# Performance work log

Hardware: AMD Instinct MI355X
Metric: run time of the kernel (lower is better)

The kernel has to match this reference:

```python
import jax, jax.numpy as jnp
import numpy as np

ROUTINGS = 3
NUM_CAPSULE = 32
DIM_CAPSULE = 64


def squash(x, axis=-1):
    # scale = sqrt(||x||^2 + eps) / (0.5 + ||x||^2 + eps)
    sq = jnp.sum(x * x, axis=axis, keepdims=True) + 1e-7
    return (jnp.sqrt(sq) / (0.5 + sq)) * x


def setup_inputs() -> dict:
    key = jax.random.key(0)
    k1, k2 = jax.random.split(key)
    B, IN, ID = 64, 1024, 256
    u_vecs = jax.random.normal(k1, (B, IN, ID), dtype=jnp.float32)
    # nn.Linear weight [NC*DC, ID], xavier_normal init
    fan_out, fan_in = NUM_CAPSULE * DIM_CAPSULE, ID
    std = np.sqrt(2.0 / (fan_in + fan_out)).astype(np.float32)
    W = jax.random.normal(k2, (fan_out, fan_in), dtype=jnp.float32) * std
    return {"u_vecs": u_vecs, "W": W}


def reference(u_vecs, W):
    B, IN, ID = u_vecs.shape
    # Linear projection: [B, IN, NC*DC]
    u_hat = jnp.einsum('bid,od->bio', u_vecs, W)
    # -> [B, NC, IN, DC]
    u_hat = u_hat.reshape(B, IN, NUM_CAPSULE, DIM_CAPSULE).transpose(0, 2, 1, 3)

    b = jnp.zeros((B, NUM_CAPSULE, IN), dtype=u_hat.dtype)
    o = None
    for i in range(ROUTINGS):
        c = jax.nn.softmax(b, axis=1)                      # softmax over output capsules
        o = jnp.einsum('bni,bnid->bnd', c, u_hat)          # [B, NC, DC]
        if i < ROUTINGS - 1:
            # F.normalize(o, 2, -1): x / max(||x||, 1e-12)
            norm = jnp.linalg.norm(o, axis=-1, keepdims=True)
            o = o / jnp.maximum(norm, 1e-12)
            b = jnp.einsum('bnid,bnd->bni', u_hat, o)
    return squash(o)
```

## Files before the change

kernel.cpp:

```cpp
#include <hip/hip_runtime.h>
#include <math.h>


#define B   64
#define IN  1024
#define ID  256
#define NC  32
#define DC  64

__global__ __launch_bounds__(256) void k_sumu(const float* __restrict__ u,
                                              float* __restrict__ sp0) {
    const int c = blockIdx.x, b = blockIdx.y;
    const int d = threadIdx.x;
    const float* up = u + ((size_t)b * IN + (size_t)c * (IN / 8)) * ID + d;
    float acc = 0.f;
#pragma unroll 8
    for (int i = 0; i < IN / 8; ++i) acc += up[(size_t)i * ID];
    sp0[(c * B + b) * ID + d] = acc;
}

__global__ __launch_bounds__(256) void k_ot(const float* __restrict__ W,
                                            const float* __restrict__ src,
                                            float* __restrict__ tout,
                                            const int mode) {
    const int bn = blockIdx.x;
    const int b = bn / NC, n = bn % NC;
    __shared__ float s_lds[ID];
    __shared__ float o_lds[DC];
    __shared__ float on_lds[DC];
    const int tid = threadIdx.x;

    float sv = 0.f;
    if (mode == 0) {
#pragma unroll
        for (int c = 0; c < 8; ++c) sv += src[(c * B + b) * ID + tid];
        sv *= (1.0f / NC);
    } else {
#pragma unroll
        for (int c = 0; c < 8; ++c) sv += src[((size_t)(c * B + b) * NC + n) * ID + tid];
    }
    s_lds[tid] = sv;
    __syncthreads();

    const int wave = tid >> 6, lane = tid & 63;
    const float* Wn = W + (size_t)n * DC * ID;
#pragma unroll 4
    for (int r = 0; r < 16; ++r) {
        const int d = wave * 16 + r;
        const float* wrow = Wn + (size_t)d * ID;
        float p = wrow[lane]        * s_lds[lane]
                + wrow[lane + 64]   * s_lds[lane + 64]
                + wrow[lane + 128]  * s_lds[lane + 128]
                + wrow[lane + 192]  * s_lds[lane + 192];
#pragma unroll
        for (int off = 32; off > 0; off >>= 1) p += __shfl_down(p, off);
        if (lane == 0) o_lds[d] = p;
    }
    __syncthreads();

    if (mode == 2) {
        if (tid < DC) {
            float v = o_lds[tid];
            float sq = v * v;
#pragma unroll
            for (int off = 32; off > 0; off >>= 1) sq += __shfl_down(sq, off);
            sq = __shfl(sq, 0) + 1e-7f;
            const float sc = sqrtf(sq) / (0.5f + sq);
            tout[(size_t)(b * NC + n) * DC + tid] = v * sc;
        }
        return;
    }

    if (tid < DC) {
        float v = o_lds[tid];
        float sq = v * v;
#pragma unroll
        for (int off = 32; off > 0; off >>= 1) sq += __shfl_down(sq, off);
        sq = __shfl(sq, 0);
        const float inv = 1.0f / fmaxf(sqrtf(sq), 1e-12f);
        on_lds[tid] = v * inv;
    }
    __syncthreads();

    float acc = 0.f;
    const float* wc = Wn + tid;
#pragma unroll 8
    for (int d = 0; d < DC; ++d) acc += wc[(size_t)d * ID] * on_lds[d];
    tout[((size_t)b * NC + n) * ID + tid] = acc;
}

#define RTILE 128
__global__ __launch_bounds__(256) void k_route(const float* __restrict__ u,
                                               const float* __restrict__ t,
                                               float* __restrict__ sp) {
    const int it = blockIdx.x, b = blockIdx.y;
    const int iBase = it * RTILE;
    __shared__ __align__(16) float Tst[NC][ID];
    __shared__ __align__(16) float Us[2][RTILE][20];
    __shared__ __align__(16) float cl[RTILE][36];
    const int tid = threadIdx.x;

    const float* ub = u + ((size_t)b * IN + iBase) * ID;
    const float* tb = t + (size_t)b * NC * ID;

#pragma unroll
    for (int rep = 0; rep < 8; ++rep) {
        const int idx = tid + rep * 256;
        const int n = idx >> 6, c4 = idx & 63;
        const float4 v = *(const float4*)(tb + (size_t)n * ID + c4 * 4);
        const int c_sw = (c4 * 4) ^ (((n >> 2) & 7) << 2);
        *(float4*)&Tst[n][c_sw] = v;
    }

    const int q = tid >> 3;
    const int r = tid & 7;
    const int i0 = q * 4, n0 = r * 4;
    const int si0 = tid >> 2,        sk0 = tid & 3;
    const int si1 = (tid + 256) >> 2, sk1 = (tid + 256) & 3;
    const int sc0 = 4 * (sk0 ^ ((si0 >> 2) & 3));
    const int sc1 = 4 * (sk1 ^ ((si1 >> 2) & 3));
    const int qs = q & 3;

    float acc[4][4] = {{0.f}};
    float4 pre0 = *(const float4*)(ub + (size_t)si0 * ID + sk0 * 4);
    float4 pre1 = *(const float4*)(ub + (size_t)si1 * ID + sk1 * 4);

    for (int kc = 0; kc < ID / 16; ++kc) {
        const int buf = kc & 1;
        *(float4*)&Us[buf][si0][sc0] = pre0;
        *(float4*)&Us[buf][si1][sc1] = pre1;
        __syncthreads();
        if (kc < ID / 16 - 1) {
            pre0 = *(const float4*)(ub + (size_t)si0 * ID + (kc + 1) * 16 + sk0 * 4);
            pre1 = *(const float4*)(ub + (size_t)si1 * ID + (kc + 1) * 16 + sk1 * 4);
        }
#pragma unroll
        for (int k4 = 0; k4 < 4; ++k4) {
            float4 a[4], bv[4];
            const int ac = 4 * (k4 ^ qs);
#pragma unroll
            for (int ii = 0; ii < 4; ++ii) a[ii] = *(const float4*)&Us[buf][i0 + ii][ac];
            const int bc = (kc * 16 + k4 * 4) ^ (r << 2);
#pragma unroll
            for (int jj = 0; jj < 4; ++jj) bv[jj] = *(const float4*)&Tst[n0 + jj][bc];
#pragma unroll
            for (int ii = 0; ii < 4; ++ii)
#pragma unroll
                for (int jj = 0; jj < 4; ++jj)
                    acc[ii][jj] += a[ii].x * bv[jj].x + a[ii].y * bv[jj].y
                                 + a[ii].z * bv[jj].z + a[ii].w * bv[jj].w;
        }
        __syncthreads();
    }

#pragma unroll
    for (int ii = 0; ii < 4; ++ii)
        *(float4*)&cl[i0 + ii][n0] =
            make_float4(acc[ii][0], acc[ii][1], acc[ii][2], acc[ii][3]);
    __syncthreads();

    {
        const int i = tid >> 1, half = tid & 1;
        float v[16];
#pragma unroll
        for (int j = 0; j < 16; ++j) v[j] = cl[i][half * 16 + j];
        float mx = v[0];
#pragma unroll
        for (int j = 1; j < 16; ++j) mx = fmaxf(mx, v[j]);
        mx = fmaxf(mx, __shfl_xor(mx, 1));
        float sum = 0.f;
#pragma unroll
        for (int j = 0; j < 16; ++j) { v[j] = __expf(v[j] - mx); sum += v[j]; }
        sum += __shfl_xor(sum, 1);
        const float inv = 1.0f / sum;
#pragma unroll
        for (int j = 0; j < 16; ++j) cl[i][half * 16 + j] = v[j] * inv;
    }
    __syncthreads();

    const int d4 = tid & 63;
    const int ng = tid >> 6;
    float a2[8][4] = {{0.f}};
    const float* ur = ub + d4 * 4;
#pragma unroll 4
    for (int i = 0; i < RTILE; ++i) {
        const float4 uv = *(const float4*)(ur + (size_t)i * ID);
        const float4 c0 = *(const float4*)&cl[i][ng * 8];
        const float4 c1 = *(const float4*)&cl[i][ng * 8 + 4];
        const float cv[8] = {c0.x, c0.y, c0.z, c0.w, c1.x, c1.y, c1.z, c1.w};
        const float uvv[4] = {uv.x, uv.y, uv.z, uv.w};
#pragma unroll
        for (int j = 0; j < 8; ++j)
#pragma unroll
            for (int x = 0; x < 4; ++x) a2[j][x] += cv[j] * uvv[x];
    }

    float* spb = sp + (size_t)(it * B + b) * NC * ID;
#pragma unroll
    for (int j = 0; j < 8; ++j) {
        const int n = ng * 8 + j;
        *(float4*)&spb[(size_t)n * ID + d4 * 4] =
            make_float4(a2[j][0], a2[j][1], a2[j][2], a2[j][3]);
    }
}

extern "C" void kernel_launch(void* const* d_in, const int* in_sizes, int n_in,
                              void* d_out, int out_size, void* d_ws, size_t ws_size,
                              hipStream_t stream) {
    const float* u = (const float*)d_in[0];
    const float* W = (const float*)d_in[1];
    float* out = (float*)d_out;

    float* ws  = (float*)d_ws;
    float* t   = ws;
    float* sp  = t + (size_t)B * NC * ID;
    float* sp0 = sp + (size_t)8 * B * NC * ID;

    k_sumu <<<dim3(8, B), dim3(256), 0, stream>>>(u, sp0);
    k_ot   <<<dim3(B * NC), dim3(256), 0, stream>>>(W, sp0, t, 0);
    k_route<<<dim3(IN / RTILE, B), dim3(256), 0, stream>>>(u, t, sp);
    k_ot   <<<dim3(B * NC), dim3(256), 0, stream>>>(W, sp, t, 1);
    k_route<<<dim3(IN / RTILE, B), dim3(256), 0, stream>>>(u, t, sp);
    k_ot   <<<dim3(B * NC), dim3(256), 0, stream>>>(W, sp, out, 2);
}
```

Measured before the change: 236.7 us.

## Read u directly from global in routing GEMM and alias shared buffers

The routing kernel no longer stages u tiles through a double-buffered shared-memory array with per-chunk barriers. Each thread now loads its four u rows directly from global memory as float4 and keeps only the T matrix in LDS. The logits buffer is aliased onto the same LDS as T, which cuts LDS use so more blocks can run per CU (launch bounds set to 4). The trade is uncoalesced, strided global loads of u that rely on L1/L2 caching instead of explicit LDS reuse across the eight threads sharing each row.

```diff
diff --git a/kernel.cpp b/kernel.cpp
--- a/kernel.cpp
+++ b/kernel.cpp
@@ -90,14 +90,14 @@
 }
 
 #define RTILE 128
-__global__ __launch_bounds__(256) void k_route(const float* __restrict__ u,
-                                               const float* __restrict__ t,
-                                               float* __restrict__ sp) {
+__global__ __launch_bounds__(256, 4) void k_route(const float* __restrict__ u,
+                                                  const float* __restrict__ t,
+                                                  float* __restrict__ sp) {
     const int it = blockIdx.x, b = blockIdx.y;
     const int iBase = it * RTILE;
-    __shared__ __align__(16) float Tst[NC][ID];
-    __shared__ __align__(16) float Us[2][RTILE][20];
-    __shared__ __align__(16) float cl[RTILE][36];
+    __shared__ __align__(16) float smem[NC * ID];
+    float (*Tst)[ID] = (float(*)[ID])smem;
+    float (*cl)[36]  = (float(*)[36])smem;
     const int tid = threadIdx.x;
 
     const float* ub = u + ((size_t)b * IN + iBase) * ID;
@@ -108,50 +108,39 @@
         const int idx = tid + rep * 256;
         const int n = idx >> 6, c4 = idx & 63;
         const float4 v = *(const float4*)(tb + (size_t)n * ID + c4 * 4);
-        const int c_sw = (c4 * 4) ^ (((n >> 2) & 7) << 2);
-        *(float4*)&Tst[n][c_sw] = v;
-    }
+        *(float4*)&Tst[n][(c4 * 4) ^ ((n >> 2) << 2)] = v;
+    }
+    __syncthreads();
 
     const int q = tid >> 3;
     const int r = tid & 7;
     const int i0 = q * 4, n0 = r * 4;
-    const int si0 = tid >> 2,        sk0 = tid & 3;
-    const int si1 = (tid + 256) >> 2, sk1 = (tid + 256) & 3;
-    const int sc0 = 4 * (sk0 ^ ((si0 >> 2) & 3));
-    const int sc1 = 4 * (sk1 ^ ((si1 >> 2) & 3));
-    const int qs = q & 3;
-
+    const int rsw = r << 2;
     float acc[4][4] = {{0.f}};
-    float4 pre0 = *(const float4*)(ub + (size_t)si0 * ID + sk0 * 4);
-    float4 pre1 = *(const float4*)(ub + (size_t)si1 * ID + sk1 * 4);
-
-    for (int kc = 0; kc < ID / 16; ++kc) {
-        const int buf = kc & 1;
-        *(float4*)&Us[buf][si0][sc0] = pre0;
-        *(float4*)&Us[buf][si1][sc1] = pre1;
-        __syncthreads();
-        if (kc < ID / 16 - 1) {
-            pre0 = *(const float4*)(ub + (size_t)si0 * ID + (kc + 1) * 16 + sk0 * 4);
-            pre1 = *(const float4*)(ub + (size_t)si1 * ID + (kc + 1) * 16 + sk1 * 4);
-        }
-#pragma unroll
-        for (int k4 = 0; k4 < 4; ++k4) {
-            float4 a[4], bv[4];
-            const int ac = 4 * (k4 ^ qs);
-#pragma unroll
-            for (int ii = 0; ii < 4; ++ii) a[ii] = *(const float4*)&Us[buf][i0 + ii][ac];
-            const int bc = (kc * 16 + k4 * 4) ^ (r << 2);
-#pragma unroll
-            for (int jj = 0; jj < 4; ++jj) bv[jj] = *(const float4*)&Tst[n0 + jj][bc];
-#pragma unroll
-            for (int ii = 0; ii < 4; ++ii)
-#pragma unroll
-                for (int jj = 0; jj < 4; ++jj)
-                    acc[ii][jj] += a[ii].x * bv[jj].x + a[ii].y * bv[jj].y
-                                 + a[ii].z * bv[jj].z + a[ii].w * bv[jj].w;
-        }
-        __syncthreads();
-    }
+    const float* up0 = ub + (size_t)(i0 + 0) * ID;
+    const float* up1 = ub + (size_t)(i0 + 1) * ID;
+    const float* up2 = ub + (size_t)(i0 + 2) * ID;
+    const float* up3 = ub + (size_t)(i0 + 3) * ID;
+
+#pragma unroll 4
+    for (int k4 = 0; k4 < ID / 4; ++k4) {
+        float4 a[4];
+        a[0] = *(const float4*)(up0 + k4 * 4);
+        a[1] = *(const float4*)(up1 + k4 * 4);
+        a[2] = *(const float4*)(up2 + k4 * 4);
+        a[3] = *(const float4*)(up3 + k4 * 4);
+        const int bc = (k4 * 4) ^ rsw;
+        float4 bv[4];
+#pragma unroll
+        for (int jj = 0; jj < 4; ++jj) bv[jj] = *(const float4*)&Tst[n0 + jj][bc];
+#pragma unroll
+        for (int ii = 0; ii < 4; ++ii)
+#pragma unroll
+            for (int jj = 0; jj < 4; ++jj)
+                acc[ii][jj] += a[ii].x * bv[jj].x + a[ii].y * bv[jj].y
+                             + a[ii].z * bv[jj].z + a[ii].w * bv[jj].w;
+    }
+    __syncthreads();
 
 #pragma unroll
     for (int ii = 0; ii < 4; ++ii)
```

Result: no change. 240.1 us (+1.4%).
